# Kernel tuning notes

Hardware: AMD Instinct MI355X
Metric: run time of the kernel (lower is better)

The kernel has to match this reference:

```python
import jax, jax.numpy as jnp
import numpy as np


def setup_inputs() -> dict:
    key = jax.random.key(0)
    kq, kk, kv = jax.random.split(key, 3)
    G, B, H, S, D = 4, 2, 16, 1024, 64  # ring size, batch, heads, seq_local, dim_head
    shape = (G, B, H, S, D)
    q = jax.random.normal(kq, shape, dtype=jnp.float32)
    k = jax.random.normal(kk, shape, dtype=jnp.float32)
    v = jax.random.normal(kv, shape, dtype=jnp.float32)
    return {"q": q, "k": k, "v": v}


def reference(q, k, v):
    """Ring attention with online (logsumexp) softmax merge.

    q, k, v: [G, B, H, S_local, D] where G is the number of ring participants.
    Each ring step: every participant attends its local Q against the currently
    visiting K/V chunk, then K/V chunks rotate around the ring (roll on axis 0).
    """
    G = q.shape[0]
    scale = 1.0 / np.sqrt(q.shape[-1]).astype(np.float32)
    out = jnp.zeros_like(q)
    # running logsumexp per query: [G, B, H, S, 1]
    lse = jnp.full(q.shape[:-1] + (1,), -jnp.inf, dtype=q.dtype)
    cur_k, cur_v = k, v
    for ring_step in range(G):
        # [G,B,H,Sq,Sk] chunk attention scores
        scores = jnp.einsum('gbhqd,gbhkd->gbhqk', q, cur_k) * scale
        chunk_max = scores.max(axis=-1, keepdims=True)
        chunk_exp = jnp.exp(scores - chunk_max)
        chunk_sum = chunk_exp.sum(axis=-1, keepdims=True)
        chunk_lse = chunk_max + jnp.log(chunk_sum)
        chunk_out = jnp.einsum('gbhqk,gbhkd->gbhqd', chunk_exp / chunk_sum, cur_v)
        # online merge via logaddexp rescaling
        new_lse = jnp.logaddexp(lse, chunk_lse)
        out = out * jnp.exp(lse - new_lse) + chunk_out * jnp.exp(chunk_lse - new_lse)
        lse = new_lse
        if ring_step < G - 1:
            # next_k[i] = current_k[i-1]  ->  roll +1 along ring axis
            cur_k = jnp.roll(cur_k, 1, axis=0)
            cur_v = jnp.roll(cur_v, 1, axis=0)
    return out
```

## Files before the change

### kernel.cpp

```cpp
#include <hip/hip_runtime.h>
#include <stdint.h>


#define RG 4
#define RB 2
#define RH 16
#define RS 1024
#define RD 64

using bf16x8 = __attribute__((ext_vector_type(8))) short;
using bf16x4 = __attribute__((ext_vector_type(4))) short;
using f16x8  = __attribute__((ext_vector_type(8))) _Float16;
using f32x4  = __attribute__((ext_vector_type(4))) float;
using u32x2  = __attribute__((ext_vector_type(2))) uint32_t;
using u32x4  = __attribute__((ext_vector_type(4))) uint32_t;

#if __has_builtin(__builtin_amdgcn_mfma_f32_16x16x16_bf16)
#define MFMA_PV(a, b, c) __builtin_amdgcn_mfma_f32_16x16x16_bf16(a, b, c, 0, 0, 0)
#else
#define MFMA_PV(a, b, c) __builtin_amdgcn_mfma_f32_16x16x16bf16_1k(a, b, c, 0, 0, 0)
#endif

#if __has_builtin(__builtin_amdgcn_exp2f)
#define EXP2F(x) __builtin_amdgcn_exp2f(x)
#else
#define EXP2F(x) exp2f(x)
#endif

__device__ inline uint16_t f2bf(float x) {
    uint32_t u = __float_as_uint(x);
    u += 0x7fffu + ((u >> 16) & 1u);
    return (uint16_t)(u >> 16);
}
__device__ inline float bf2f(uint16_t b) {
    return __uint_as_float(((uint32_t)b) << 16);
}
__device__ inline uint32_t pkbf2(float lo, float hi) {
    uint32_t a = __float_as_uint(lo) + 0x8000u;
    uint32_t b = __float_as_uint(hi) + 0x8000u;
    return (a >> 16) | (b & 0xffff0000u);
}
__device__ inline uint32_t pkh2(float lo, float hi) {
#if __has_builtin(__builtin_amdgcn_cvt_pkrtz)
    return __builtin_bit_cast(uint32_t, __builtin_amdgcn_cvt_pkrtz(lo, hi));
#else
    union { _Float16 h[2]; uint32_t u; } r;
    r.h[0] = (_Float16)lo; r.h[1] = (_Float16)hi;
    return r.u;
#endif
}
__device__ inline uint4 pack8(const uint16_t* h) {
    uint4 r;
    r.x = (uint32_t)h[0] | ((uint32_t)h[1] << 16);
    r.y = (uint32_t)h[2] | ((uint32_t)h[3] << 16);
    r.z = (uint32_t)h[4] | ((uint32_t)h[5] << 16);
    r.w = (uint32_t)h[6] | ((uint32_t)h[7] << 16);
    return r;
}

__device__ inline void glds16(const uint16_t* g, uint16_t* lbase, int lane) {
#if __has_builtin(__builtin_amdgcn_global_load_lds)
    __builtin_amdgcn_global_load_lds(
        (const __attribute__((address_space(1))) uint32_t*)g,
        (__attribute__((address_space(3))) uint32_t*)lbase, 16, 0, 0);
#else
    *(uint4*)(lbase + lane * 8) = *(const uint4*)g;
#endif
}

__global__ __launch_bounds__(256)
void prep_kv(const float* __restrict__ k, const float* __restrict__ v,
             uint16_t* __restrict__ kf, uint16_t* __restrict__ vf) {
    const int bid = blockIdx.x;
    const int t = threadIdx.x;
    const size_t base = (size_t)bid * (64 * RD);

    {
        uint4 o[2];
#pragma unroll
        for (int si = 0; si < 2; ++si) {
            const int s  = 2 * t + si;
            const int ks = s >> 8, nt = (s >> 6) & 3, ln = s & 63;
            const int key = nt * 16 + (ln & 15);
            const int d   = ks * 32 + (ln >> 4) * 8;
            const float* sp = k + base + (size_t)key * RD + d;
            float4 a0 = ((const float4*)sp)[0];
            float4 a1 = ((const float4*)sp)[1];
            o[si].x = pkh2(a0.x, a0.y); o[si].y = pkh2(a0.z, a0.w);
            o[si].z = pkh2(a1.x, a1.y); o[si].w = pkh2(a1.z, a1.w);
        }
        uint16_t* dst = kf + (size_t)bid * 4096 + t * 16;
        ((uint4*)dst)[0] = o[0]; ((uint4*)dst)[1] = o[1];
    }
    {
        const int s0 = 2 * t;
        const int dt = s0 >> 7, b = (s0 >> 6) & 1, ln = s0 & 63;
        const int c = ln & 15, qd = ln >> 4;
        const int d = dt * 16 + c;
        float x0[8], x1[8];
#pragma unroll
        for (int j = 0; j < 8; ++j) {
            const int key = b * 32 + ((j >> 2) << 4) + qd * 4 + (j & 3);
            float2 xv = *(const float2*)(v + base + (size_t)key * RD + d);
            x0[j] = xv.x; x1[j] = xv.y;
        }
        uint4 o0, o1;
        o0.x = pkh2(x0[0], x0[1]); o0.y = pkh2(x0[2], x0[3]);
        o0.z = pkh2(x0[4], x0[5]); o0.w = pkh2(x0[6], x0[7]);
        o1.x = pkh2(x1[0], x1[1]); o1.y = pkh2(x1[2], x1[3]);
        o1.z = pkh2(x1[4], x1[5]); o1.w = pkh2(x1[6], x1[7]);
        uint16_t* dst = vf + (size_t)bid * 4096 + t * 16;
        ((uint4*)dst)[0] = o0; ((uint4*)dst)[1] = o1;
    }
}

constexpr int TILE_SH = 4096;
constexpr int BUF_SH  = 2 * TILE_SH;
constexpr int SMEM4   = 2 * BUF_SH;

__device__ inline void stage_tile(uint16_t* smem, const uint16_t* kf_g,
                                  const uint16_t* vf_g, size_t tb,
                                  int dbuf, int tid, int wave, int lane) {
    const uint16_t* gk = kf_g + tb;
    const uint16_t* gv = vf_g + tb;
    uint16_t* lk = smem + dbuf * BUF_SH + wave * 512;
    uint16_t* lv = smem + dbuf * BUF_SH + TILE_SH + wave * 512;
    glds16(gk + (size_t)tid * 8,         lk,        lane);
    glds16(gk + (size_t)(256 + tid) * 8, lk + 2048, lane);
    glds16(gv + (size_t)tid * 8,         lv,        lane);
    glds16(gv + (size_t)(256 + tid) * 8, lv + 2048, lane);
}

__global__ __launch_bounds__(256, 4)
void ring_attn_mfma6(const float* __restrict__ q, const uint16_t* __restrict__ kf_g,
                     const uint16_t* __restrict__ vf_g, float* __restrict__ out) {
    __shared__ __attribute__((aligned(16))) uint16_t smem[SMEM4];

    const int tid  = threadIdx.x;
    const int wave = tid >> 6;
    const int lane = tid & 63;
    const int quad = lane >> 4;
    const int col  = lane & 15;

    {
        uint32_t* sw = (uint32_t*)smem;
#pragma unroll
        for (int i = 0; i < SMEM4 / 2 / 256; ++i) sw[i * 256 + tid] = 0u;
    }
    __syncthreads();

    const int bid   = blockIdx.x;
    const int head  = bid & 127;
    const int qtile = bid >> 7;
    const int bh    = head & 31;

    const size_t hcq = (size_t)head * (RS * RD);
    const int qbase  = qtile * 128 + wave * 32;

    const float sc = 0.125f * 1.44269504088896340736f;

    stage_tile(smem, kf_g, vf_g, (size_t)(bh * 16) * TILE_SH, 0, tid, wave, lane);

    f16x8 qf[2][2];
#pragma unroll
    for (int mt = 0; mt < 2; ++mt)
#pragma unroll
        for (int ks = 0; ks < 2; ++ks) {
            const float* qp = q + hcq + (size_t)(qbase + mt * 16 + col) * RD + ks * 32 + quad * 8;
            float4 t0 = ((const float4*)qp)[0];
            float4 t1 = ((const float4*)qp)[1];
            u32x4 w = {pkh2(t0.x * sc, t0.y * sc), pkh2(t0.z * sc, t0.w * sc),
                       pkh2(t1.x * sc, t1.y * sc), pkh2(t1.z * sc, t1.w * sc)};
            qf[mt][ks] = __builtin_bit_cast(f16x8, w);
        }

    f32x4 oacc[2][4];
#pragma unroll
    for (int mt = 0; mt < 2; ++mt)
#pragma unroll
        for (int dt = 0; dt < 4; ++dt) oacc[mt][dt] = (f32x4){0.f, 0.f, 0.f, 0.f};
    float lrun[2] = {0.f, 0.f};

    __syncthreads();

    int cur = 0;
    for (int it = 0; it < (RG * RS) / 64; ++it) {
        const bool pre = (it < (RG * RS) / 64 - 1);
        if (pre) {
            const int nit = it + 1;
            const size_t tb =
                (size_t)((((nit >> 4) * 32 + bh) << 4) + (nit & 15)) * TILE_SH;
            stage_tile(smem, kf_g, vf_g, tb, cur ^ 1, tid, wave, lane);
        }

        const uint16_t* kbuf = &smem[cur * BUF_SH];
        const uint16_t* vbuf = kbuf + TILE_SH;

        f32x4 sacc[2][4];
#pragma unroll
        for (int mt = 0; mt < 2; ++mt)
#pragma unroll
            for (int nt = 0; nt < 4; ++nt) sacc[mt][nt] = (f32x4){0.f, 0.f, 0.f, 0.f};
        __builtin_amdgcn_s_setprio(1);
#pragma unroll
        for (int nt = 0; nt < 4; ++nt) {
            f16x8 kfr[2];
            kfr[0] = *(const f16x8*)&kbuf[(size_t)((0 * 4 + nt) * 64 + lane) * 8];
            kfr[1] = *(const f16x8*)&kbuf[(size_t)((1 * 4 + nt) * 64 + lane) * 8];
#pragma unroll
            for (int mt = 0; mt < 2; ++mt)
#pragma unroll
                for (int ks = 0; ks < 2; ++ks)
                    sacc[mt][nt] = __builtin_amdgcn_mfma_f32_16x16x32_f16(kfr[ks], qf[mt][ks], sacc[mt][nt], 0, 0, 0);
        }
        __builtin_amdgcn_s_setprio(0);

        f16x8 pf[2][2];
#pragma unroll
        for (int mt = 0; mt < 2; ++mt) {
            float ls = 0.f;
            uint32_t w[4][2];
#pragma unroll
            for (int nt = 0; nt < 4; ++nt) {
                float p0 = EXP2F(sacc[mt][nt][0]);
                float p1 = EXP2F(sacc[mt][nt][1]);
                float p2 = EXP2F(sacc[mt][nt][2]);
                float p3 = EXP2F(sacc[mt][nt][3]);
                ls += (p0 + p1) + (p2 + p3);
                w[nt][0] = pkh2(p0, p1);
                w[nt][1] = pkh2(p2, p3);
            }
            u32x4 b0 = {w[0][0], w[0][1], w[1][0], w[1][1]};
            u32x4 b1 = {w[2][0], w[2][1], w[3][0], w[3][1]};
            pf[mt][0] = __builtin_bit_cast(f16x8, b0);
            pf[mt][1] = __builtin_bit_cast(f16x8, b1);
            lrun[mt] += ls;
        }

        __builtin_amdgcn_s_setprio(1);
#pragma unroll
        for (int dt = 0; dt < 4; ++dt)
#pragma unroll
            for (int b = 0; b < 2; ++b) {
                f16x8 vfr = *(const f16x8*)&vbuf[(size_t)((dt * 2 + b) * 64 + lane) * 8];
#pragma unroll
                for (int mt = 0; mt < 2; ++mt)
                    oacc[mt][dt] = __builtin_amdgcn_mfma_f32_16x16x32_f16(vfr, pf[mt][b], oacc[mt][dt], 0, 0, 0);
            }
        __builtin_amdgcn_s_setprio(0);

        __syncthreads();
        cur ^= 1;
    }

#pragma unroll
    for (int mt = 0; mt < 2; ++mt) {
        lrun[mt] += __shfl_xor(lrun[mt], 16);
        lrun[mt] += __shfl_xor(lrun[mt], 32);
        const float inv = 1.0f / lrun[mt];
        const int qrow = qbase + mt * 16 + col;
#pragma unroll
        for (int dt = 0; dt < 4; ++dt) {
            float4 st;
            st.x = oacc[mt][dt][0] * inv;
            st.y = oacc[mt][dt][1] * inv;
            st.z = oacc[mt][dt][2] * inv;
            st.w = oacc[mt][dt][3] * inv;
            *(float4*)&out[hcq + (size_t)qrow * RD + dt * 16 + quad * 4] = st;
        }
    }
}

__global__ __launch_bounds__(256)
void prep_vt(const float* __restrict__ v, uint16_t* __restrict__ vt) {
    __shared__ uint16_t tl[64 * 72];
    const int bid = blockIdx.x;
    const int hc = bid >> 4, kt = bid & 15;
    const size_t base = (size_t)hc * (RS * RD);
    const int t = threadIdx.x;
    const int row = t >> 2;
    const int seg = (t & 3) * 16;

    const float* src = v + base + (size_t)(kt * 64 + row) * RD + seg;
    uint16_t hb[16];
#pragma unroll
    for (int i = 0; i < 4; ++i) {
        float4 x = ((const float4*)src)[i];
        hb[4 * i + 0] = f2bf(x.x); hb[4 * i + 1] = f2bf(x.y);
        hb[4 * i + 2] = f2bf(x.z); hb[4 * i + 3] = f2bf(x.w);
    }
    uint16_t* d = &tl[row * 72 + seg];
    ((uint4*)d)[0] = pack8(hb); ((uint4*)d)[1] = pack8(hb + 8);
    __syncthreads();

    uint16_t ob[16];
#pragma unroll
    for (int i = 0; i < 16; ++i) ob[i] = tl[(seg + i) * 72 + row];
    uint16_t* dst = vt + base + (size_t)row * RS + kt * 64 + seg;
    ((uint4*)dst)[0] = pack8(ob); ((uint4*)dst)[1] = pack8(ob + 8);
}

constexpr int KSTR   = 72;
constexpr int OFF_K  = 0;
constexpr int OFF_VT = 64 * KSTR;
constexpr int SMEM2  = 2 * 64 * KSTR;

__global__ __launch_bounds__(256, 4)
void ring_attn_mfma3(const float* __restrict__ q, const float* __restrict__ k_g,
                     const uint16_t* __restrict__ vt_g, float* __restrict__ out) {
    __shared__ __attribute__((aligned(16))) uint16_t smem[SMEM2];

    const int tid  = threadIdx.x;
    const int wave = tid >> 6;
    const int lane = tid & 63;
    const int quad = lane >> 4;
    const int col  = lane & 15;

    {
        uint32_t* sw = (uint32_t*)smem;
#pragma unroll
        for (int i = 0; i < SMEM2 / 2 / 256; ++i) sw[i * 256 + tid] = 0u;
    }

    const int bid   = blockIdx.x;
    const int head  = bid & 127;
    const int qtile = bid >> 7;
    const int bh    = head & 31;

    const size_t hcq = (size_t)head * (RS * RD);
    const int qbase  = qtile * 128 + wave * 32;

    const float sc = 0.125f * 1.44269504088896340736f;

    bf16x8 qh[2][2], ql[2][2];
#pragma unroll
    for (int mt = 0; mt < 2; ++mt)
#pragma unroll
        for (int ks = 0; ks < 2; ++ks) {
            const float* qp = q + hcq + (size_t)(qbase + mt * 16 + col) * RD + ks * 32 + quad * 8;
            float4 t0 = ((const float4*)qp)[0];
            float4 t1 = ((const float4*)qp)[1];
            float xs[8] = {t0.x, t0.y, t0.z, t0.w, t1.x, t1.y, t1.z, t1.w};
            bf16x8 hv, lv;
#pragma unroll
            for (int j = 0; j < 8; ++j) {
                float x = xs[j] * sc;
                uint16_t hb = f2bf(x);
                hv[j] = (short)hb;
                lv[j] = (short)f2bf(x - bf2f(hb));
            }
            qh[mt][ks] = hv;
            ql[mt][ks] = lv;
        }

    f32x4 oacc[2][4];
#pragma unroll
    for (int mt = 0; mt < 2; ++mt)
#pragma unroll
        for (int dt = 0; dt < 4; ++dt) oacc[mt][dt] = (f32x4){0.f, 0.f, 0.f, 0.f};
    float lrun[2] = {0.f, 0.f};

    const int srow = tid >> 2;
    const int sseg = (tid & 3) * 16;

    for (int it = 0; it < (RG * RS) / 64; ++it) {
        const int gp = it >> 4, ktile = it & 15;
        const size_t cbase = (size_t)(gp * 32 + bh) * (RS * RD);

        __syncthreads();
        {
            const float* kp = k_g + cbase + (size_t)(ktile * 64 + srow) * RD + sseg;
            float4 a0 = ((const float4*)kp)[0];
            float4 a1 = ((const float4*)kp)[1];
            float4 a2 = ((const float4*)kp)[2];
            float4 a3 = ((const float4*)kp)[3];
            uint4 w0, w1;
            w0.x = pkbf2(a0.x, a0.y); w0.y = pkbf2(a0.z, a0.w);
            w0.z = pkbf2(a1.x, a1.y); w0.w = pkbf2(a1.z, a1.w);
            w1.x = pkbf2(a2.x, a2.y); w1.y = pkbf2(a2.z, a2.w);
            w1.z = pkbf2(a3.x, a3.y); w1.w = pkbf2(a3.z, a3.w);
            uint16_t* d0 = &smem[OFF_K + srow * KSTR + sseg];
            ((uint4*)d0)[0] = w0;
            ((uint4*)d0)[1] = w1;
            const uint16_t* s2 = vt_g + cbase + (size_t)srow * RS + ktile * 64 + sseg;
            uint16_t* d2 = &smem[OFF_VT + srow * KSTR + sseg];
            ((uint4*)d2)[0] = ((const uint4*)s2)[0];
            ((uint4*)d2)[1] = ((const uint4*)s2)[1];
        }
        __syncthreads();

        f32x4 sacc[2][4];
#pragma unroll
        for (int mt = 0; mt < 2; ++mt)
#pragma unroll
            for (int nt = 0; nt < 4; ++nt) sacc[mt][nt] = (f32x4){0.f, 0.f, 0.f, 0.f};
#pragma unroll
        for (int nt = 0; nt < 4; ++nt) {
            bf16x8 kf[2];
#pragma unroll
            for (int ks = 0; ks < 2; ++ks)
                kf[ks] = *(const bf16x8*)&smem[OFF_K + (nt * 16 + col) * KSTR + ks * 32 + quad * 8];
#pragma unroll
            for (int mt = 0; mt < 2; ++mt)
#pragma unroll
                for (int ks = 0; ks < 2; ++ks) {
                    sacc[mt][nt] = __builtin_amdgcn_mfma_f32_16x16x32_bf16(kf[ks], qh[mt][ks], sacc[mt][nt], 0, 0, 0);
                    sacc[mt][nt] = __builtin_amdgcn_mfma_f32_16x16x32_bf16(kf[ks], ql[mt][ks], sacc[mt][nt], 0, 0, 0);
                }
        }

        bf16x4 pf[2][4];
#pragma unroll
        for (int mt = 0; mt < 2; ++mt) {
            float ls = 0.f;
#pragma unroll
            for (int nt = 0; nt < 4; ++nt) {
                float p0 = EXP2F(sacc[mt][nt][0]);
                float p1 = EXP2F(sacc[mt][nt][1]);
                float p2 = EXP2F(sacc[mt][nt][2]);
                float p3 = EXP2F(sacc[mt][nt][3]);
                ls += (p0 + p1) + (p2 + p3);
                u32x2 t;
                t[0] = pkbf2(p0, p1);
                t[1] = pkbf2(p2, p3);
                pf[mt][nt] = __builtin_bit_cast(bf16x4, t);
            }
            lrun[mt] += ls;
        }

#pragma unroll
        for (int dt = 0; dt < 4; ++dt) {
            bf16x4 vf[4];
#pragma unroll
            for (int nt = 0; nt < 4; ++nt)
                vf[nt] = *(const bf16x4*)&smem[OFF_VT + (dt * 16 + col) * KSTR + nt * 16 + quad * 4];
#pragma unroll
            for (int mt = 0; mt < 2; ++mt)
#pragma unroll
                for (int nt = 0; nt < 4; ++nt)
                    oacc[mt][dt] = MFMA_PV(vf[nt], pf[mt][nt], oacc[mt][dt]);
        }
    }

#pragma unroll
    for (int mt = 0; mt < 2; ++mt) {
        lrun[mt] += __shfl_xor(lrun[mt], 16);
        lrun[mt] += __shfl_xor(lrun[mt], 32);
        const float inv = 1.0f / lrun[mt];
        const int qrow = qbase + mt * 16 + col;
#pragma unroll
        for (int dt = 0; dt < 4; ++dt) {
            float4 st;
            st.x = oacc[mt][dt][0] * inv;
            st.y = oacc[mt][dt][1] * inv;
            st.z = oacc[mt][dt][2] * inv;
            st.w = oacc[mt][dt][3] * inv;
            *(float4*)&out[hcq + (size_t)qrow * RD + dt * 16 + quad * 4] = st;
        }
    }
}

extern "C" void kernel_launch(void* const* d_in, const int* in_sizes, int n_in,
                              void* d_out, int out_size, void* d_ws, size_t ws_size,
                              hipStream_t stream) {
    const float* q = (const float*)d_in[0];
    const float* k = (const float*)d_in[1];
    const float* v = (const float*)d_in[2];
    float* out = (float*)d_out;

    const size_t NEL = (size_t)RG * RB * RH * RS * RD;
    const size_t need2 = 2 * NEL * sizeof(uint16_t);
    const size_t need1 = NEL * sizeof(uint16_t);

    if (ws_size >= need2) {
        uint16_t* kf = (uint16_t*)d_ws;
        uint16_t* vf = kf + NEL;
        prep_kv<<<2048, 256, 0, stream>>>(k, v, kf, vf);
        ring_attn_mfma6<<<1024, 256, 0, stream>>>(q, kf, vf, out);
    } else if (ws_size >= need1) {
        uint16_t* vt = (uint16_t*)d_ws;
        prep_vt<<<2048, 256, 0, stream>>>(v, vt);
        ring_attn_mfma3<<<1024, 256, 0, stream>>>(q, k, vt, out);
    } else {
        uint16_t* vt = (uint16_t*)d_ws;
        prep_vt<<<2048, 256, 0, stream>>>(v, vt);
        ring_attn_mfma3<<<1024, 256, 0, stream>>>(q, k, vt, out);
    }
}
```

Baseline: 259.8 us.

## Software-pipeline QK of the next tile with softmax/PV of current tile

Restructures the main loop so that the QK^T MFMAs for tile t+1 are issued before the exp/pack and PV work of tile t. This lets matrix-core work overlap with the transcendental and VALU work. K now uses two buffers and V uses three, with prefetch running two tiles ahead. The cost is more LDS, more live score registers, and launch bounds lowered from 4 to 3 waves per SIMD, which may reduce occupancy.

```diff
diff --git a/kernel.cpp b/kernel.cpp
--- a/kernel.cpp
+++ b/kernel.cpp
@@ -115,26 +115,13 @@
 }
 
 constexpr int TILE_SH = 4096;
-constexpr int BUF_SH  = 2 * TILE_SH;
-constexpr int SMEM4   = 2 * BUF_SH;
-
-__device__ inline void stage_tile(uint16_t* smem, const uint16_t* kf_g,
-                                  const uint16_t* vf_g, size_t tb,
-                                  int dbuf, int tid, int wave, int lane) {
-    const uint16_t* gk = kf_g + tb;
-    const uint16_t* gv = vf_g + tb;
-    uint16_t* lk = smem + dbuf * BUF_SH + wave * 512;
-    uint16_t* lv = smem + dbuf * BUF_SH + TILE_SH + wave * 512;
-    glds16(gk + (size_t)tid * 8,         lk,        lane);
-    glds16(gk + (size_t)(256 + tid) * 8, lk + 2048, lane);
-    glds16(gv + (size_t)tid * 8,         lv,        lane);
-    glds16(gv + (size_t)(256 + tid) * 8, lv + 2048, lane);
-}
-
-__global__ __launch_bounds__(256, 4)
-void ring_attn_mfma6(const float* __restrict__ q, const uint16_t* __restrict__ kf_g,
+constexpr int NT      = (RG * RS) / 64;
+constexpr int SMEM5   = 5 * TILE_SH;
+
+__global__ __launch_bounds__(256, 3)
+void ring_attn_mfma7(const float* __restrict__ q, const uint16_t* __restrict__ kf_g,
                      const uint16_t* __restrict__ vf_g, float* __restrict__ out) {
-    __shared__ __attribute__((aligned(16))) uint16_t smem[SMEM4];
+    __shared__ __attribute__((aligned(16))) uint16_t smem[SMEM5];
 
     const int tid  = threadIdx.x;
     const int wave = tid >> 6;
@@ -145,7 +132,7 @@
     {
         uint32_t* sw = (uint32_t*)smem;
 #pragma unroll
-        for (int i = 0; i < SMEM4 / 2 / 256; ++i) sw[i * 256 + tid] = 0u;
+        for (int i = 0; i < SMEM5 / 2 / 256; ++i) sw[i * 256 + tid] = 0u;
     }
     __syncthreads();
 
@@ -159,7 +146,21 @@
 
     const float sc = 0.125f * 1.44269504088896340736f;
 
-    stage_tile(smem, kf_g, vf_g, (size_t)(bh * 16) * TILE_SH, 0, tid, wave, lane);
+    auto stage = [&](int it, int kslot, int vslot) {
+        const size_t tb =
+            (size_t)((((it >> 4) * 32 + bh) << 4) + (it & 15)) * TILE_SH;
+        const uint16_t* gk = kf_g + tb;
+        const uint16_t* gv = vf_g + tb;
+        uint16_t* lk = smem + kslot * TILE_SH + wave * 512;
+        uint16_t* lv = smem + (2 + vslot) * TILE_SH + wave * 512;
+        glds16(gk + (size_t)tid * 8,         lk,        lane);
+        glds16(gk + (size_t)(256 + tid) * 8, lk + 2048, lane);
+        glds16(gv + (size_t)tid * 8,         lv,        lane);
+        glds16(gv + (size_t)(256 + tid) * 8, lv + 2048, lane);
+    };
+
+    stage(0, 0, 0);
+    stage(1, 1, 1);
 
     f16x8 qf[2][2];
 #pragma unroll
@@ -181,39 +182,37 @@
         for (int dt = 0; dt < 4; ++dt) oacc[mt][dt] = (f32x4){0.f, 0.f, 0.f, 0.f};
     float lrun[2] = {0.f, 0.f};
 
+    const f32x4 ZV = {0.f, 0.f, 0.f, 0.f};
+
+    auto qk_tile = [&](f32x4 (&sN)[2][4], const uint16_t* kbuf) {
+#pragma unroll
+        for (int nt = 0; nt < 4; ++nt) {
+            f16x8 k0 = *(const f16x8*)&kbuf[(size_t)((0 * 4 + nt) * 64 + lane) * 8];
+            f16x8 k1 = *(const f16x8*)&kbuf[(size_t)((1 * 4 + nt) * 64 + lane) * 8];
+#pragma unroll
+            for (int mt = 0; mt < 2; ++mt) {
+                f32x4 acc = __builtin_amdgcn_mfma_f32_16x16x32_f16(k0, qf[mt][0], ZV, 0, 0, 0);
+                sN[mt][nt] = __builtin_amdgcn_mfma_f32_16x16x32_f16(k1, qf[mt][1], acc, 0, 0, 0);
+            }
+        }
+    };
+
     __syncthreads();
 
-    int cur = 0;
-    for (int it = 0; it < (RG * RS) / 64; ++it) {
-        const bool pre = (it < (RG * RS) / 64 - 1);
-        if (pre) {
-            const int nit = it + 1;
-            const size_t tb =
-                (size_t)((((nit >> 4) * 32 + bh) << 4) + (nit & 15)) * TILE_SH;
-            stage_tile(smem, kf_g, vf_g, tb, cur ^ 1, tid, wave, lane);
-        }
-
-        const uint16_t* kbuf = &smem[cur * BUF_SH];
-        const uint16_t* vbuf = kbuf + TILE_SH;
-
-        f32x4 sacc[2][4];
-#pragma unroll
-        for (int mt = 0; mt < 2; ++mt)
-#pragma unroll
-            for (int nt = 0; nt < 4; ++nt) sacc[mt][nt] = (f32x4){0.f, 0.f, 0.f, 0.f};
-        __builtin_amdgcn_s_setprio(1);
-#pragma unroll
-        for (int nt = 0; nt < 4; ++nt) {
-            f16x8 kfr[2];
-            kfr[0] = *(const f16x8*)&kbuf[(size_t)((0 * 4 + nt) * 64 + lane) * 8];
-            kfr[1] = *(const f16x8*)&kbuf[(size_t)((1 * 4 + nt) * 64 + lane) * 8];
-#pragma unroll
-            for (int mt = 0; mt < 2; ++mt)
-#pragma unroll
-                for (int ks = 0; ks < 2; ++ks)
-                    sacc[mt][nt] = __builtin_amdgcn_mfma_f32_16x16x32_f16(kfr[ks], qf[mt][ks], sacc[mt][nt], 0, 0, 0);
-        }
-        __builtin_amdgcn_s_setprio(0);
+    f32x4 sA[2][4], sB[2][4];
+    qk_tile(sA, smem);
+    __syncthreads();
+
+    auto run_iter = [&](int t, f32x4 (&sC)[2][4], f32x4 (&sN)[2][4], int vbt) {
+        if (t + 2 < NT) {
+            int vs = vbt + 2; if (vs >= 3) vs -= 3;
+            stage(t + 2, t & 1, vs);
+        }
+        if (t + 1 < NT) {
+            __builtin_amdgcn_s_setprio(1);
+            qk_tile(sN, smem + ((t + 1) & 1) * TILE_SH);
+            __builtin_amdgcn_s_setprio(0);
+        }
 
         f16x8 pf[2][2];
 #pragma unroll
@@ -222,10 +221,10 @@
             uint32_t w[4][2];
 #pragma unroll
             for (int nt = 0; nt < 4; ++nt) {
-                float p0 = EXP2F(sacc[mt][nt][0]);
-                float p1 = EXP2F(sacc[mt][nt][1]);
-                float p2 = EXP2F(sacc[mt][nt][2]);
-                float p3 = EXP2F(sacc[mt][nt][3]);
+                float p0 = EXP2F(sC[mt][nt][0]);
+                float p1 = EXP2F(sC[mt][nt][1]);
+                float p2 = EXP2F(sC[mt][nt][2]);
+                float p3 = EXP2F(sC[mt][nt][3]);
                 ls += (p0 + p1) + (p2 + p3);
                 w[nt][0] = pkh2(p0, p1);
                 w[nt][1] = pkh2(p2, p3);
@@ -237,6 +236,7 @@
             lrun[mt] += ls;
         }
 
+        const uint16_t* vbuf = smem + (2 + vbt) * TILE_SH;
         __builtin_amdgcn_s_setprio(1);
 #pragma unroll
         for (int dt = 0; dt < 4; ++dt)
@@ -250,7 +250,12 @@
         __builtin_amdgcn_s_setprio(0);
 
         __syncthreads();
-        cur ^= 1;
+    };
+
+    int vb = 0;
+    for (int t = 0; t < NT; t += 2) {
+        run_iter(t,     sA, sB, vb); vb = (vb == 2) ? 0 : vb + 1;
+        run_iter(t + 1, sB, sA, vb); vb = (vb == 2) ? 0 : vb + 1;
     }
 
 #pragma unroll
@@ -476,7 +481,7 @@
         uint16_t* kf = (uint16_t*)d_ws;
         uint16_t* vf = kf + NEL;
         prep_kv<<<2048, 256, 0, stream>>>(k, v, kf, vf);
-        ring_attn_mfma6<<<1024, 256, 0, stream>>>(q, kf, vf, out);
+        ring_attn_mfma7<<<1024, 256, 0, stream>>>(q, kf, vf, out);
     } else if (ws_size >= need1) {
         uint16_t* vt = (uint16_t*)d_ws;
         prep_vt<<<2048, 256, 0, stream>>>(v, vt);
```

After: 312.5 us. 20.3% more time.
